# Kernel tuning notes

Measured on AMD Instinct MI355X. Metric: run time of the kernel, lower is better.

The kernel has to match this reference:

```python
import jax, jax.numpy as jnp
import numpy as np

LC = 3  # number of multigrid levels


def injection1d(v):
    # fine -> coarse: take every other point, L -> (L+1)//2
    return v[..., ::2]


def interp1d(v):
    # coarse -> fine linear interpolation, L -> 2L-1
    B, C, N = v.shape
    out = jnp.zeros((B, C, 2 * N - 1), dtype=v.dtype)
    out = out.at[..., ::2].set(v)
    out = out.at[..., 1::2].set(0.5 * (v[..., :-1] + v[..., 1:]))
    return out


def mlp(xc, w1, c1, w2, c2, w3, c3):
    # pointwise (Conv1d kernel_size=1) MLP: [1 -> 64 -> 64 -> 1] with tanh
    h = jnp.tanh(jnp.einsum('oc,bcn->bon', w1, xc) + c1[:, None])
    h = jnp.tanh(jnp.einsum('oc,bcn->bon', w2, h) + c2[:, None])
    return jnp.einsum('oc,bcn->bon', w3, h) + c3[:, None]


def kernel_approximation(x, W1, b1, W2, b2, W3, b3):
    for _ in range(LC):
        x = injection1d(x)
    n = x.shape[-1]
    a = None
    n_ = 0
    for j in range(LC):
        band = mlp(x, W1[j], b1[j], W2[j], b2[j], W3[j], b3[j])  # (B, 1, n)
        if j == 0:
            a = band
            n_ = (n - 1) // 4
        else:
            a = a.at[..., n_:n_ + n].set(band)
            n_ = n_ * 2
        a = interp1d(a)
    return a  # (B, 1, 2N-1)


def toeplitz_mvp(a, u):
    # a: (B, 1, 2N-1) kernel values k(d), u: (B, 1, N)
    # w_i = sum_j a[N-1 + i - j] u_j  via circular FFT convolution of length 2N-1
    n = u.shape[-1]
    L = 2 * n - 1
    A = jnp.fft.rfft(a, n=L)
    U = jnp.fft.rfft(u, n=L)
    w = jnp.fft.irfft(A * U, n=L)
    return w[..., n - 1:]  # (B, 1, N)


def setup_inputs() -> dict:
    key = jax.random.key(0)
    ks = jax.random.split(key, 10)
    B, N = 1024, 8193
    u = jax.random.normal(ks[0], (B, 1, N), dtype=jnp.float32)
    # displacement coordinates in [-1, 1], length 2N-1, same for each batch row
    grid = jnp.linspace(-1.0, 1.0, 2 * N - 1, dtype=jnp.float32)
    x = jnp.broadcast_to(grid[None, None, :], (B, 1, 2 * N - 1)).astype(jnp.float32)
    # per-level MLP params, stacked over LC levels
    W1 = jax.random.normal(ks[1], (LC, 64, 1), dtype=jnp.float32) * 1.0
    b1 = jax.random.normal(ks[2], (LC, 64), dtype=jnp.float32) * 0.1
    W2 = jax.random.normal(ks[3], (LC, 64, 64), dtype=jnp.float32) * (1.0 / np.sqrt(64))
    b2 = jax.random.normal(ks[4], (LC, 64), dtype=jnp.float32) * 0.1
    W3 = jax.random.normal(ks[5], (LC, 1, 64), dtype=jnp.float32) * (1.0 / np.sqrt(64))
    b3 = jax.random.normal(ks[6], (LC, 1), dtype=jnp.float32) * 0.1
    return {"u": u, "x": x, "W1": W1, "b1": b1, "W2": W2, "b2": b2, "W3": W3, "b3": b3}


def reference(u, x, W1, b1, W2, b2, W3, b3):
    a = kernel_approximation(x, W1, b1, W2, b2, W3, b3)
    w = toeplitz_mvp(a, u)
    return w
```

## Files before the change

### kernel.cpp

```cpp
#include <hip/hip_runtime.h>

#define NN  8193
#define FN  16384
#define NTHR 1024

#define ZIDX(i) ((i) + ((i) >> 4) + ((i) >> 6) + ((i) >> 10))
#define ZPAD 17680

#define OFF_BANDS 0u
#define OFF_AF32  24832u
#define OFF_AHAT  90624u
#define OFF_TW    221952u
#define OFF_TAU   320256u

__device__ __forceinline__ float2 cmul(float2 a, float2 b) {
  return make_float2(a.x * b.x - a.y * b.y, a.x * b.y + a.y * b.x);
}
__device__ __forceinline__ float2 cadd(float2 a, float2 b) { return make_float2(a.x + b.x, a.y + b.y); }
__device__ __forceinline__ float2 csub(float2 a, float2 b) { return make_float2(a.x - b.x, a.y - b.y); }

__device__ __forceinline__ int rev4_14(int k) {
  int r = 0;
  #pragma unroll
  for (int i = 0; i < 7; ++i) { r = (r << 2) | (k & 3); k >>= 2; }
  return r;
}

template<int Q, int M, bool INV>
__device__ __forceinline__ void stage4(float2* Z, const float2* __restrict__ tw,
                                       int tid) {
  constexpr int ZO = (Q == 4096) ? 4420 : (Q == 1024) ? 1105 : (Q == 256) ? 276
                   : (Q == 64)   ? 69   : (Q == 16)   ? 17   : 4;
  #pragma unroll 1
  for (int r = 0; r < FN / 4 / NTHR; ++r) {
    const int idx = tid + r * NTHR;
    const int j  = idx & (Q - 1);
    const int b1 = idx / Q;
    const int z0 = ZIDX(b1 * 4 * Q + j);
    float2 w1 = tw[j * M];
    if (INV) w1.y = -w1.y;
    const float2 w2 = cmul(w1, w1);
    const float2 w3 = cmul(w1, w2);
    if (!INV) {
      float2 c0 = Z[z0], c1 = Z[z0 + ZO], c2 = Z[z0 + 2 * ZO], c3 = Z[z0 + 3 * ZO];
      float2 t0 = cadd(c0, c2), t1 = csub(c0, c2), t2 = cadd(c1, c3);
      float2 t3 = make_float2(c1.y - c3.y, -(c1.x - c3.x));
      Z[z0]          = cadd(t0, t2);
      Z[z0 + ZO]     = cmul(w1, cadd(t1, t3));
      Z[z0 + 2 * ZO] = cmul(w2, csub(t0, t2));
      Z[z0 + 3 * ZO] = cmul(w3, csub(t1, t3));
    } else {
      float2 u0 = Z[z0];
      float2 u1 = cmul(w1, Z[z0 + ZO]);
      float2 u2 = cmul(w2, Z[z0 + 2 * ZO]);
      float2 u3 = cmul(w3, Z[z0 + 3 * ZO]);
      float2 s0 = cadd(u0, u2), s1 = csub(u0, u2), s2 = cadd(u1, u3);
      float2 s3 = make_float2(-(u1.y - u3.y), u1.x - u3.x);
      Z[z0]          = cadd(s0, s2);
      Z[z0 + ZO]     = cadd(s1, s3);
      Z[z0 + 2 * ZO] = csub(s0, s2);
      Z[z0 + 3 * ZO] = csub(s1, s3);
    }
  }
}

__device__ __forceinline__ void s6_fwd(float2* Z, int tid) {
  #pragma unroll 1
  for (int m = tid; m < FN / 4; m += NTHR) {
    const int zb = 4 * m + (m >> 2) + (m >> 4) + (m >> 8);
    float2 c0 = Z[zb], c1 = Z[zb + 1], c2 = Z[zb + 2], c3 = Z[zb + 3];
    float2 t0 = cadd(c0, c2), t1 = csub(c0, c2), t2 = cadd(c1, c3);
    float2 t3 = make_float2(c1.y - c3.y, -(c1.x - c3.x));
    Z[zb]     = cadd(t0, t2);
    Z[zb + 1] = cadd(t1, t3);
    Z[zb + 2] = csub(t0, t2);
    Z[zb + 3] = csub(t1, t3);
  }
}
__device__ __forceinline__ void s6_inv(float2* Z, int tid) {
  #pragma unroll 1
  for (int m = tid; m < FN / 4; m += NTHR) {
    const int zb = 4 * m + (m >> 2) + (m >> 4) + (m >> 8);
    float2 u0 = Z[zb], u1 = Z[zb + 1], u2 = Z[zb + 2], u3 = Z[zb + 3];
    float2 s0 = cadd(u0, u2), s1 = csub(u0, u2), s2 = cadd(u1, u3);
    float2 s3 = make_float2(-(u1.y - u3.y), u1.x - u3.x);
    Z[zb]     = cadd(s0, s2);
    Z[zb + 1] = cadd(s1, s3);
    Z[zb + 2] = csub(s0, s2);
    Z[zb + 3] = csub(s1, s3);
  }
}

__device__ void fft_fwd(float2* Z, const float2* __restrict__ tw, int tid) {
  stage4<4096, 1, false>(Z, tw, tid);   __syncthreads();
  stage4<1024, 4, false>(Z, tw, tid);   __syncthreads();
  stage4<256, 16, false>(Z, tw, tid);   __syncthreads();
  stage4<64, 64, false>(Z, tw, tid);    __syncthreads();
  stage4<16, 256, false>(Z, tw, tid);   __syncthreads();
  stage4<4, 1024, false>(Z, tw, tid);   __syncthreads();
  s6_fwd(Z, tid);                       __syncthreads();
}
__device__ void fft_inv(float2* Z, const float2* __restrict__ tw, int tid) {
  s6_inv(Z, tid);                       __syncthreads();
  stage4<4, 1024, true>(Z, tw, tid);    __syncthreads();
  stage4<16, 256, true>(Z, tw, tid);    __syncthreads();
  stage4<64, 64, true>(Z, tw, tid);     __syncthreads();
  stage4<256, 16, true>(Z, tw, tid);    __syncthreads();
  stage4<1024, 4, true>(Z, tw, tid);    __syncthreads();
  stage4<4096, 1, true>(Z, tw, tid);    __syncthreads();
}

__global__ void k_tw(float2* __restrict__ tw, float2* __restrict__ tau) {
  const int i = blockIdx.x * 256 + threadIdx.x;
  if (i < 4096) {
    const float ang = -6.283185307179586f * (float)i / 16384.0f;
    tw[i] = make_float2(cosf(ang), sinf(ang));
  }
  if (i <= 16384) {
    const float ang = -3.1415926535897932f * (float)i / 16384.0f;
    tau[i] = make_float2(cosf(ang), sinf(ang));
  }
}

__global__ void k_bands(const float* __restrict__ x,
                        const float* __restrict__ W1, const float* __restrict__ b1,
                        const float* __restrict__ W2, const float* __restrict__ b2,
                        const float* __restrict__ W3, const float* __restrict__ b3,
                        float* __restrict__ bands) {
  const int j = blockIdx.y;
  __shared__ float w2s[4096];
  __shared__ float w1s[64], b1s[64], b2s[64], w3s[64];
  for (int i = threadIdx.x; i < 4096; i += 256) w2s[i] = W2[j * 4096 + i];
  if (threadIdx.x < 64) {
    w1s[threadIdx.x] = W1[j * 64 + threadIdx.x];
    b1s[threadIdx.x] = b1[j * 64 + threadIdx.x];
    b2s[threadIdx.x] = b2[j * 64 + threadIdx.x];
    w3s[threadIdx.x] = W3[j * 64 + threadIdx.x];
  }
  __syncthreads();
  const int k = blockIdx.x * 256 + threadIdx.x;
  if (k >= 2049) return;
  const float xc = x[8 * k];
  float h1[64];
  #pragma unroll
  for (int o = 0; o < 64; ++o) h1[o] = tanhf(w1s[o] * xc + b1s[o]);
  float outv = b3[j];
  for (int o = 0; o < 64; ++o) {
    float a0 = 0.f, a1 = 0.f, a2 = 0.f, a3 = 0.f;
    #pragma unroll
    for (int c = 0; c < 64; c += 4) {
      a0 += w2s[o * 64 + c] * h1[c];
      a1 += w2s[o * 64 + c + 1] * h1[c + 1];
      a2 += w2s[o * 64 + c + 2] * h1[c + 2];
      a3 += w2s[o * 64 + c + 3] * h1[c + 3];
    }
    outv += w3s[o] * tanhf(b2s[o] + ((a0 + a1) + (a2 + a3)));
  }
  bands[j * 2049 + k] = outv;
}

__global__ void k_interp(const float* __restrict__ bands, float* __restrict__ af32) {
  __shared__ float s1[4097];
  __shared__ float s2[8193];
  const int tid = threadIdx.x;
  const float* bd0 = bands;
  const float* bd1 = bands + 2049;
  const float* bd2 = bands + 2 * 2049;
  for (int i = tid; i < 4097; i += 1024) {
    float v = (i & 1) ? 0.5f * (bd0[i >> 1] + bd0[(i >> 1) + 1]) : bd0[i >> 1];
    if (i >= 512 && i < 2561) v = bd1[i - 512];
    s1[i] = v;
  }
  __syncthreads();
  for (int i = tid; i < 8193; i += 1024) {
    float v = (i & 1) ? 0.5f * (s1[i >> 1] + s1[(i >> 1) + 1]) : s1[i >> 1];
    if (i >= 1024 && i < 3073) v = bd2[i - 1024];
    s2[i] = v;
  }
  __syncthreads();
  for (int i = tid; i < 16385; i += 1024) {
    float v = (i & 1) ? 0.5f * (s2[i >> 1] + s2[(i >> 1) + 1]) : s2[i >> 1];
    af32[i] = v;
  }
}

__global__ __launch_bounds__(NTHR, 4) void k_ahat(const float* __restrict__ af32,
                                                  const float2* __restrict__ tw,
                                                  const float2* __restrict__ tau,
                                                  float2* __restrict__ Ahat) {
  __shared__ float2 Z[ZPAD];
  const int tid = threadIdx.x;
  for (int n = tid; n < FN; n += NTHR) {
    float2 v = make_float2(0.f, 0.f);
    if (n < 8192)       v = make_float2(af32[2 * n], af32[2 * n + 1]);
    else if (n == 8192) v = make_float2(af32[16384], 0.f);
    Z[ZIDX(n)] = v;
  }
  __syncthreads();
  fft_fwd(Z, tw, tid);
  const float sc = 1.0f / 16384.0f;
  for (int k = tid; k <= 16384; k += NTHR) {
    float2 A;
    if (k == 0) {
      float2 z0 = Z[ZIDX(0)];
      A = make_float2((z0.x + z0.y) * sc, 0.f);
    } else if (k == 16384) {
      float2 z0 = Z[ZIDX(0)];
      A = make_float2((z0.x - z0.y) * sc, 0.f);
    } else if (k == 8192) {
      float2 z8 = Z[ZIDX(rev4_14(8192))];
      A = make_float2(z8.x * sc, -z8.y * sc);
    } else {
      const int kc = 16384 - k;
      float2 Zk = Z[ZIDX(rev4_14(k))];
      float2 Zc = Z[ZIDX(rev4_14(kc))];
      float2 E = make_float2(0.5f * (Zk.x + Zc.x), 0.5f * (Zk.y - Zc.y));
      float2 D = make_float2(Zk.x - Zc.x, Zk.y + Zc.y);
      float2 O = make_float2(0.5f * D.y, -0.5f * D.x);
      float2 tk = tau[k];
      float2 tO = cmul(tk, O);
      A = make_float2((E.x + tO.x) * sc, (E.y + tO.y) * sc);
    }
    Ahat[k] = A;
  }
}

__global__ __launch_bounds__(NTHR, 4) void k_conv(const float* __restrict__ u,
                                                  const float2* __restrict__ Ahat,
                                                  const float2* __restrict__ tw,
                                                  const float2* __restrict__ tau,
                                                  float* __restrict__ out) {
  __shared__ float2 Z[ZPAD];
  const int tid = threadIdx.x;
  const int b = blockIdx.x;
  const float* ub = u + (size_t)b * NN;

  for (int n = tid; n < FN; n += NTHR) {
    float2 v = make_float2(0.f, 0.f);
    if (n == 0)          v = make_float2(ub[8192], 0.f);
    else if (n >= 12288) {
      const int m = n - 12288;
      v = make_float2(ub[2 * m], ub[2 * m + 1]);
    }
    Z[ZIDX(n)] = v;
  }
  __syncthreads();

  fft_fwd(Z, tw, tid);

  for (int i = tid; i < 8192; i += NTHR) {
    if (i == 0) {
      float2 z0 = Z[ZIDX(0)];
      float X0 = z0.x + z0.y;
      float XN = z0.x - z0.y;
      float Y0 = X0 * Ahat[0].x;
      float YN = XN * Ahat[16384].x;
      Z[ZIDX(0)] = make_float2(0.5f * (Y0 + YN), 0.5f * (Y0 - YN));
      const int r8 = rev4_14(8192);
      float2 z8 = Z[ZIDX(r8)];
      float2 X8 = make_float2(z8.x, -z8.y);
      float2 Y8 = cmul(X8, Ahat[8192]);
      Z[ZIDX(r8)] = make_float2(Y8.x, -Y8.y);
    } else {
      const int k = i, kc = 16384 - i;
      const int rk = ZIDX(rev4_14(k)), rkc = ZIDX(rev4_14(kc));
      float2 Zk = Z[rk], Zc = Z[rkc];
      float2 E = make_float2(0.5f * (Zk.x + Zc.x), 0.5f * (Zk.y - Zc.y));
      float2 D = make_float2(Zk.x - Zc.x, Zk.y + Zc.y);
      float2 O = make_float2(0.5f * D.y, -0.5f * D.x);
      float2 tk = tau[k];
      float2 tO = cmul(tk, O);
      float2 Xk = make_float2(E.x + tO.x, E.y + tO.y);
      float2 Xc = make_float2(E.x - tO.x, -(E.y - tO.y));
      float2 Yk = cmul(Xk, Ahat[k]);
      float2 Y2 = cmul(Xc, Ahat[kc]);
      float2 Ep = make_float2(0.5f * (Yk.x + Y2.x), 0.5f * (Yk.y - Y2.y));
      float2 D2 = make_float2(0.5f * (Yk.x - Y2.x), 0.5f * (Yk.y + Y2.y));
      float2 tb = make_float2(tk.x, -tk.y);
      float2 Op = cmul(tb, D2);
      Z[rk]  = make_float2(Ep.x - Op.y, Ep.y + Op.x);
      Z[rkc] = make_float2(Ep.x + Op.y, -Ep.y + Op.x);
    }
  }
  __syncthreads();

  fft_inv(Z, tw, tid);

  float* ob = out + (size_t)b * NN;
  for (int n = tid; n <= 4096; n += NTHR) {
    float2 w = Z[ZIDX(n)];
    if (n < 4096) {
      ob[2 * n]     = w.x;
      ob[2 * n + 1] = w.y;
    } else {
      ob[8192] = w.x;
    }
  }
}

extern "C" void kernel_launch(void* const* d_in, const int* in_sizes, int n_in,
                              void* d_out, int out_size, void* d_ws, size_t ws_size,
                              hipStream_t stream) {
  (void)in_sizes; (void)n_in; (void)out_size; (void)ws_size;
  const float* u  = (const float*)d_in[0];
  const float* x  = (const float*)d_in[1];
  const float* W1 = (const float*)d_in[2];
  const float* b1 = (const float*)d_in[3];
  const float* W2 = (const float*)d_in[4];
  const float* b2 = (const float*)d_in[5];
  const float* W3 = (const float*)d_in[6];
  const float* b3 = (const float*)d_in[7];
  float* out = (float*)d_out;
  char*  ws  = (char*)d_ws;

  float*  bands = (float*)(ws + OFF_BANDS);
  float*  af32  = (float*)(ws + OFF_AF32);
  float2* Ahat  = (float2*)(ws + OFF_AHAT);
  float2* tw    = (float2*)(ws + OFF_TW);
  float2* tau   = (float2*)(ws + OFF_TAU);

  k_tw<<<65, 256, 0, stream>>>(tw, tau);
  k_bands<<<dim3(9, 3), 256, 0, stream>>>(x, W1, b1, W2, b2, W3, b3, bands);
  k_interp<<<1, 1024, 0, stream>>>(bands, af32);
  k_ahat<<<1, NTHR, 0, stream>>>(af32, tw, tau, Ahat);
  k_conv<<<1024, NTHR, 0, stream>>>(u, Ahat, tw, tau, out);
}
```

Measured before the change: 215.3 us.

## Fuse first/last FFT radix-4 stages with global load/store and exploit zero padding

Folds the first forward radix-4 stage into the global-memory load loop, so the mostly-zero padded input is butterflied directly from registers without first being written to shared memory. Folds the last inverse stage into the output store, computing only the outputs that are needed. The pointwise spectral multiply loop now iterates in bit-reversed storage order for better shared-memory locality. This removes a full shared-memory pass and two barriers per FFT, at the cost of more specialized and intricate index logic.

```diff
diff --git a/kernel.cpp b/kernel.cpp
--- a/kernel.cpp
+++ b/kernel.cpp
@@ -29,8 +29,8 @@
 template<int Q, int M, bool INV>
 __device__ __forceinline__ void stage4(float2* Z, const float2* __restrict__ tw,
                                        int tid) {
-  constexpr int ZO = (Q == 4096) ? 4420 : (Q == 1024) ? 1105 : (Q == 256) ? 276
-                   : (Q == 64)   ? 69   : (Q == 16)   ? 17   : 4;
+  constexpr int ZO = (Q == 1024) ? 1105 : (Q == 256) ? 276
+                   : (Q == 64)   ? 69   : (Q == 16)  ? 17  : 4;
   #pragma unroll 1
   for (int r = 0; r < FN / 4 / NTHR; ++r) {
     const int idx = tid + r * NTHR;
@@ -91,8 +91,7 @@
   }
 }
 
-__device__ void fft_fwd(float2* Z, const float2* __restrict__ tw, int tid) {
-  stage4<4096, 1, false>(Z, tw, tid);   __syncthreads();
+__device__ void fft_fwd_rest(float2* Z, const float2* __restrict__ tw, int tid) {
   stage4<1024, 4, false>(Z, tw, tid);   __syncthreads();
   stage4<256, 16, false>(Z, tw, tid);   __syncthreads();
   stage4<64, 64, false>(Z, tw, tid);    __syncthreads();
@@ -100,14 +99,13 @@
   stage4<4, 1024, false>(Z, tw, tid);   __syncthreads();
   s6_fwd(Z, tid);                       __syncthreads();
 }
-__device__ void fft_inv(float2* Z, const float2* __restrict__ tw, int tid) {
+__device__ void fft_inv_rest(float2* Z, const float2* __restrict__ tw, int tid) {
   s6_inv(Z, tid);                       __syncthreads();
   stage4<4, 1024, true>(Z, tw, tid);    __syncthreads();
   stage4<16, 256, true>(Z, tw, tid);    __syncthreads();
   stage4<64, 64, true>(Z, tw, tid);     __syncthreads();
   stage4<256, 16, true>(Z, tw, tid);    __syncthreads();
   stage4<1024, 4, true>(Z, tw, tid);    __syncthreads();
-  stage4<4096, 1, true>(Z, tw, tid);    __syncthreads();
 }
 
 __global__ void k_tw(float2* __restrict__ tw, float2* __restrict__ tau) {
@@ -190,14 +188,25 @@
                                                   float2* __restrict__ Ahat) {
   __shared__ float2 Z[ZPAD];
   const int tid = threadIdx.x;
-  for (int n = tid; n < FN; n += NTHR) {
-    float2 v = make_float2(0.f, 0.f);
-    if (n < 8192)       v = make_float2(af32[2 * n], af32[2 * n + 1]);
-    else if (n == 8192) v = make_float2(af32[16384], 0.f);
-    Z[ZIDX(n)] = v;
-  }
-  __syncthreads();
-  fft_fwd(Z, tw, tid);
+  #pragma unroll 1
+  for (int r = 0; r < 4; ++r) {
+    const int j = tid + r * NTHR;
+    const int z0 = ZIDX(j);
+    float2 c0 = make_float2(af32[2 * j], af32[2 * j + 1]);
+    float2 c1 = make_float2(af32[2 * j + 8192], af32[2 * j + 8193]);
+    float2 c2 = (j == 0) ? make_float2(af32[16384], 0.f) : make_float2(0.f, 0.f);
+    float2 w1 = tw[j];
+    float2 w2 = cmul(w1, w1), w3 = cmul(w1, w2);
+    float2 t0 = cadd(c0, c2), t1 = csub(c0, c2);
+    float2 t2 = c1;
+    float2 t3 = make_float2(c1.y, -c1.x);
+    Z[z0]           = cadd(t0, t2);
+    Z[z0 + 4420]    = cmul(w1, cadd(t1, t3));
+    Z[z0 + 2*4420]  = cmul(w2, csub(t0, t2));
+    Z[z0 + 3*4420]  = cmul(w3, csub(t1, t3));
+  }
+  __syncthreads();
+  fft_fwd_rest(Z, tw, tid);
   const float sc = 1.0f / 16384.0f;
   for (int k = tid; k <= 16384; k += NTHR) {
     float2 A;
@@ -235,35 +244,42 @@
   const int b = blockIdx.x;
   const float* ub = u + (size_t)b * NN;
 
-  for (int n = tid; n < FN; n += NTHR) {
-    float2 v = make_float2(0.f, 0.f);
-    if (n == 0)          v = make_float2(ub[8192], 0.f);
-    else if (n >= 12288) {
-      const int m = n - 12288;
-      v = make_float2(ub[2 * m], ub[2 * m + 1]);
-    }
-    Z[ZIDX(n)] = v;
-  }
-  __syncthreads();
-
-  fft_fwd(Z, tw, tid);
+  #pragma unroll 1
+  for (int r = 0; r < 4; ++r) {
+    const int j = tid + r * NTHR;
+    const int z0 = ZIDX(j);
+    float2 c3 = make_float2(ub[2 * j], ub[2 * j + 1]);
+    float2 c0 = (j == 0) ? make_float2(ub[8192], 0.f) : make_float2(0.f, 0.f);
+    float2 w1 = tw[j];
+    float2 w2 = cmul(w1, w1), w3 = cmul(w1, w2);
+    float2 ic3 = make_float2(-c3.y, c3.x);
+    Z[z0]           = cadd(c0, c3);
+    Z[z0 + 4420]    = cmul(w1, cadd(c0, ic3));
+    Z[z0 + 2*4420]  = cmul(w2, csub(c0, c3));
+    Z[z0 + 3*4420]  = cmul(w3, csub(c0, ic3));
+  }
+  __syncthreads();
+
+  fft_fwd_rest(Z, tw, tid);
 
   for (int i = tid; i < 8192; i += NTHR) {
-    if (i == 0) {
+    const int mm = ((i >> 1) << 2) | (i & 1);
+    if (mm == 0) {
       float2 z0 = Z[ZIDX(0)];
       float X0 = z0.x + z0.y;
       float XN = z0.x - z0.y;
       float Y0 = X0 * Ahat[0].x;
       float YN = XN * Ahat[16384].x;
       Z[ZIDX(0)] = make_float2(0.5f * (Y0 + YN), 0.5f * (Y0 - YN));
-      const int r8 = rev4_14(8192);
-      float2 z8 = Z[ZIDX(r8)];
+      const int r8 = ZIDX(2);
+      float2 z8 = Z[r8];
       float2 X8 = make_float2(z8.x, -z8.y);
       float2 Y8 = cmul(X8, Ahat[8192]);
-      Z[ZIDX(r8)] = make_float2(Y8.x, -Y8.y);
+      Z[r8] = make_float2(Y8.x, -Y8.y);
     } else {
-      const int k = i, kc = 16384 - i;
-      const int rk = ZIDX(rev4_14(k)), rkc = ZIDX(rev4_14(kc));
+      const int k = rev4_14(mm);
+      const int kc = 16384 - k;
+      const int rk = ZIDX(mm), rkc = ZIDX(rev4_14(kc));
       float2 Zk = Z[rk], Zc = Z[rkc];
       float2 E = make_float2(0.5f * (Zk.x + Zc.x), 0.5f * (Zk.y - Zc.y));
       float2 D = make_float2(Zk.x - Zc.x, Zk.y + Zc.y);
@@ -284,16 +300,27 @@
   }
   __syncthreads();
 
-  fft_inv(Z, tw, tid);
+  fft_inv_rest(Z, tw, tid);
 
   float* ob = out + (size_t)b * NN;
-  for (int n = tid; n <= 4096; n += NTHR) {
-    float2 w = Z[ZIDX(n)];
-    if (n < 4096) {
-      ob[2 * n]     = w.x;
-      ob[2 * n + 1] = w.y;
-    } else {
-      ob[8192] = w.x;
+  #pragma unroll 1
+  for (int r = 0; r < 4; ++r) {
+    const int j = tid + r * NTHR;
+    const int z0 = ZIDX(j);
+    float2 w1 = tw[j]; w1.y = -w1.y;
+    float2 w2 = cmul(w1, w1), w3 = cmul(w1, w2);
+    float2 u0 = Z[z0];
+    float2 u1 = cmul(w1, Z[z0 + 4420]);
+    float2 u2 = cmul(w2, Z[z0 + 2*4420]);
+    float2 u3 = cmul(w3, Z[z0 + 3*4420]);
+    float2 s0 = cadd(u0, u2), s2 = cadd(u1, u3);
+    float2 zj = cadd(s0, s2);
+    ob[2 * j]     = zj.x;
+    ob[2 * j + 1] = zj.y;
+    if (j == 0) {
+      float2 s1 = csub(u0, u2);
+      float2 s3 = make_float2(-(u1.y - u3.y), u1.x - u3.x);
+      ob[8192] = s1.x + s3.x;
     }
   }
 }
```

Measured after the change: 275.1 us. 27.8% more time.
